# Performance work log

Hardware: AMD Instinct MI355X
Metric: run time of the kernel (lower is better)

## Reference

```python
import jax, jax.numpy as jnp
import numpy as np

D = 512      # d_model
P = 128      # proj_len
H = 8        # nhead
MID = 24     # middle_dim (hardcoded in module)
HD = MID // H    # head_dim = 3
HDV = D // H     # head_dim_v = 64
SCALE = HD ** -0.5   # scaling == pscaling since head_dim == phead_dim


def setup_inputs() -> dict:
    key = jax.random.key(0)
    ks = jax.random.split(key, 12)
    L, B = 2048, 16
    def w(k, o, i):
        return jax.random.normal(k, (o, i), jnp.float32) * 0.02
    def b(o):
        return jnp.zeros((o,), jnp.float32)
    return {
        "x": jax.random.normal(ks[0], (L, B, D), jnp.float32),
        "px": jax.random.normal(ks[1], (P, B, D), jnp.float32),
        "mask": jax.random.randint(ks[2], (B, L), 0, 2).astype(bool),
        "Wpq": w(ks[3], MID, D), "bpq": b(MID),
        "Wq": w(ks[4], MID, D), "bq": b(MID),
        "Wql": w(ks[5], P * H, D), "bql": b(P * H),
        "Wpk": w(ks[6], MID, D), "bpk": b(MID),
        "Wpv": w(ks[7], D, D), "bpv": b(D),
        "Wk": w(ks[8], MID, D), "bk": b(MID),
        "Wv": w(ks[9], D, D), "bv": b(D),
        "Wo": w(ks[10], D, D), "bo": b(D),
        "gamma": jnp.ones((D,), jnp.float32),
        "beta": jnp.zeros((D,), jnp.float32),
    }


def _layernorm(x, g, b, eps=1e-5):
    m = x.mean(-1, keepdims=True)
    v = ((x - m) ** 2).mean(-1, keepdims=True)
    return (x - m) / jnp.sqrt(v + eps) * g + b


def reference(x, px, mask, Wpq, bpq, Wq, bq, Wql, bql, Wpk, bpk, Wpv, bpv,
              Wk, bk, Wv, bv, Wo, bo, gamma, beta):
    L, B, _ = x.shape
    BH = B * H
    # ---- stage 1: compress length L -> P via projected attention ----
    pk = (x @ Wpk.T + bpk).reshape(L, BH, HD)     # [L, BH, hd]
    pv = (x @ Wpv.T + bpv).reshape(L, BH, HDV)    # [L, BH, hdv]
    pq = (px @ Wpq.T + bpq).reshape(P, BH, HD) * SCALE
    pqk = jnp.einsum('pnh,lnh->npl', pq, pk)      # [BH, P, L]
    pqk = pqk.reshape(B, H, P, L)
    pqk = jnp.where(mask[:, None, None, :], -jnp.inf, pqk).reshape(BH, P, L)
    pqk = jax.nn.softmax(pqk, axis=-1)            # dropout1 omitted (eval)
    pc = jnp.einsum('npl,lnv->npv', pqk, pv)      # [BH, P, hdv]
    pc = pc.transpose(1, 0, 2).reshape(P, B, D)   # compressed context
    # ---- stage 2: attention within compressed length P ----
    q_len = (x @ Wql.T + bql).reshape(L, BH, P).transpose(1, 0, 2)  # [BH, L, P]
    k = (pc @ Wk.T + bk).reshape(P, BH, HD).transpose(1, 0, 2)      # [BH, P, hd]
    v = (pc @ Wv.T + bv).reshape(P, BH, HDV).transpose(1, 0, 2)     # [BH, P, hdv]
    q = ((pc @ Wq.T + bq) * SCALE).reshape(P, BH, HD).transpose(1, 0, 2)
    aw = jax.nn.softmax(q @ k.transpose(0, 2, 1), axis=-1)  # [BH, P, P], dropout2 omitted
    attn = aw @ v                                            # [BH, P, hdv]
    attn = attn.transpose(1, 0, 2).reshape(P, B, D)
    attn = _layernorm(attn, gamma, beta)
    attn = attn.reshape(P, BH, HDV).transpose(1, 0, 2)       # [BH, P, hdv]
    # ---- stage 3: re-expand P -> L via learned length softmax ----
    ql = jax.nn.softmax(q_len, axis=-1)                      # dropout3 omitted
    out = (ql @ attn).transpose(1, 0, 2).reshape(L, B, D)
    return (out @ Wo.T + bo, pc)
```

## Files before the change

kernel.cpp:

```cpp
#include <hip/hip_runtime.h>
#include <cstdint>

#define L_    2048
#define B_    16
#define D_    512
#define P_    128
#define H_    8
#define MID_  24
#define HD_   3
#define HDV_  64
#define BH_   128
#define SCALE_ 0.57735026918962576f
#define S1C   4
#define S1L   (L_ / S1C)

typedef short  short8  __attribute__((ext_vector_type(8)));
typedef short  short4v __attribute__((ext_vector_type(4)));
typedef float  f32x4   __attribute__((ext_vector_type(4)));

__device__ __forceinline__ short f2bf(float f) {
    unsigned u = __builtin_bit_cast(unsigned, f);
    unsigned r = (u + 0x7fffu + ((u >> 16) & 1u)) >> 16;
    return (short)(unsigned short)r;
}

__device__ __forceinline__ float block_reduce_sum_256(float v, volatile float* scratch) {
#pragma unroll
    for (int o = 32; o > 0; o >>= 1) v += __shfl_down(v, o, 64);
    int wid = threadIdx.x >> 6;
    if ((threadIdx.x & 63) == 0) scratch[wid] = v;
    __syncthreads();
    if (threadIdx.x == 0) scratch[4] = scratch[0] + scratch[1] + scratch[2] + scratch[3];
    __syncthreads();
    return scratch[4];
}

__global__ __launch_bounds__(256) void cvt_bf16(
    const float* __restrict__ src, short* __restrict__ dst, int n4)
{
    int i = blockIdx.x * 256 + threadIdx.x;
    if (i < n4) {
        float4 v = reinterpret_cast<const float4*>(src)[i];
        short4v o;
        o[0] = f2bf(v.x); o[1] = f2bf(v.y); o[2] = f2bf(v.z); o[3] = f2bf(v.w);
        reinterpret_cast<short4v*>(dst)[i] = o;
    }
}

__global__ __launch_bounds__(256) void gemm_bias(
    const float* __restrict__ A, const float* __restrict__ W,
    const float* __restrict__ bias, float* __restrict__ C,
    int M, int N, int K, float scale)
{
    __shared__ float As[32][36];
    __shared__ float Ws[64][36];
    const int t    = threadIdx.x;
    const int row0 = blockIdx.y * 32;
    const int col0 = blockIdx.x * 64;
    const int ty = t >> 4;
    const int tx = t & 15;
    const int lr  = t >> 3;
    const int lc4 = (t & 7) * 4;

    float acc[2][4] = {{0.f,0.f,0.f,0.f},{0.f,0.f,0.f,0.f}};

    for (int kk0 = 0; kk0 < K; kk0 += 32) {
        {
            float4 a = *reinterpret_cast<const float4*>(&A[(size_t)(row0 + lr) * K + kk0 + lc4]);
            *reinterpret_cast<float4*>(&As[lr][lc4]) = a;
        }
#pragma unroll
        for (int i = 0; i < 2; ++i) {
            int wr   = i * 32 + lr;
            int wcol = col0 + wr;
            float4 w = make_float4(0.f, 0.f, 0.f, 0.f);
            if (wcol < N)
                w = *reinterpret_cast<const float4*>(&W[(size_t)wcol * K + kk0 + lc4]);
            *reinterpret_cast<float4*>(&Ws[wr][lc4]) = w;
        }
        __syncthreads();
#pragma unroll
        for (int k4 = 0; k4 < 8; ++k4) {
            float4 a0 = *reinterpret_cast<const float4*>(&As[ty * 2][k4 * 4]);
            float4 a1 = *reinterpret_cast<const float4*>(&As[ty * 2 + 1][k4 * 4]);
#pragma unroll
            for (int ci = 0; ci < 4; ++ci) {
                float4 w = *reinterpret_cast<const float4*>(&Ws[ci * 16 + tx][k4 * 4]);
                acc[0][ci] += a0.x * w.x + a0.y * w.y + a0.z * w.z + a0.w * w.w;
                acc[1][ci] += a1.x * w.x + a1.y * w.y + a1.z * w.z + a1.w * w.w;
            }
        }
        __syncthreads();
    }
#pragma unroll
    for (int ri = 0; ri < 2; ++ri) {
        int r = row0 + ty * 2 + ri;
#pragma unroll
        for (int ci = 0; ci < 4; ++ci) {
            int c = col0 + ci * 16 + tx;
            if (c < N) C[(size_t)r * N + c] = (acc[ri][ci] + bias[c]) * scale;
        }
    }
}

__global__ __launch_bounds__(256) void gemm_bias2(
    const float* __restrict__ A,
    const float* __restrict__ W0, const float* __restrict__ b0, float* __restrict__ C0, float s0,
    const float* __restrict__ W1, const float* __restrict__ b1, float* __restrict__ C1, float s1,
    int M, int N, int K)
{
    const float* W    = blockIdx.z ? W1 : W0;
    const float* bias = blockIdx.z ? b1 : b0;
    float*       C    = blockIdx.z ? C1 : C0;
    const float scale = blockIdx.z ? s1 : s0;

    __shared__ float As[32][36];
    __shared__ float Ws[64][36];
    const int t    = threadIdx.x;
    const int row0 = blockIdx.y * 32;
    const int col0 = blockIdx.x * 64;
    const int ty = t >> 4;
    const int tx = t & 15;
    const int lr  = t >> 3;
    const int lc4 = (t & 7) * 4;

    float acc[2][4] = {{0.f,0.f,0.f,0.f},{0.f,0.f,0.f,0.f}};

    for (int kk0 = 0; kk0 < K; kk0 += 32) {
        {
            float4 a = *reinterpret_cast<const float4*>(&A[(size_t)(row0 + lr) * K + kk0 + lc4]);
            *reinterpret_cast<float4*>(&As[lr][lc4]) = a;
        }
#pragma unroll
        for (int i = 0; i < 2; ++i) {
            int wr   = i * 32 + lr;
            int wcol = col0 + wr;
            float4 w = make_float4(0.f, 0.f, 0.f, 0.f);
            if (wcol < N)
                w = *reinterpret_cast<const float4*>(&W[(size_t)wcol * K + kk0 + lc4]);
            *reinterpret_cast<float4*>(&Ws[wr][lc4]) = w;
        }
        __syncthreads();
#pragma unroll
        for (int k4 = 0; k4 < 8; ++k4) {
            float4 a0 = *reinterpret_cast<const float4*>(&As[ty * 2][k4 * 4]);
            float4 a1 = *reinterpret_cast<const float4*>(&As[ty * 2 + 1][k4 * 4]);
#pragma unroll
            for (int ci = 0; ci < 4; ++ci) {
                float4 w = *reinterpret_cast<const float4*>(&Ws[ci * 16 + tx][k4 * 4]);
                acc[0][ci] += a0.x * w.x + a0.y * w.y + a0.z * w.z + a0.w * w.w;
                acc[1][ci] += a1.x * w.x + a1.y * w.y + a1.z * w.z + a1.w * w.w;
            }
        }
        __syncthreads();
    }
#pragma unroll
    for (int ri = 0; ri < 2; ++ri) {
        int r = row0 + ty * 2 + ri;
#pragma unroll
        for (int ci = 0; ci < 4; ++ci) {
            int c = col0 + ci * 16 + tx;
            if (c < N) C[(size_t)r * N + c] = (acc[ri][ci] + bias[c]) * scale;
        }
    }
}

__global__ __launch_bounds__(256) void gemm_mfma_bt(
    const float* __restrict__ A, const short* __restrict__ Wb,
    const float* __restrict__ bias, float* __restrict__ C,
    int M, int N, int K)
{
    __shared__ __align__(16) short As[128][40];
    __shared__ __align__(16) short Bs[64][40];
    const int t    = threadIdx.x;
    const int w    = t >> 6;
    const int lane = t & 63;
    const int q    = lane >> 4;
    const int l16  = lane & 15;
    const int row0 = blockIdx.y * 128;
    const int col0 = blockIdx.x * 64;

    const int ar = t >> 1;
    const int ac = (t & 1) * 16;
    const int br = t >> 2;
    const int bc = (t & 3) * 8;

    const f32x4 z = {0.f, 0.f, 0.f, 0.f};
    f32x4 acc[2][4];
#pragma unroll
    for (int i = 0; i < 2; ++i)
#pragma unroll
        for (int j = 0; j < 4; ++j) acc[i][j] = z;

    for (int kk = 0; kk < K; kk += 32) {
        {
            const float4* ap = reinterpret_cast<const float4*>(&A[(size_t)(row0 + ar) * K + kk + ac]);
            float4 v0 = ap[0], v1 = ap[1], v2 = ap[2], v3 = ap[3];
            short8 s0, s1;
            s0[0]=f2bf(v0.x); s0[1]=f2bf(v0.y); s0[2]=f2bf(v0.z); s0[3]=f2bf(v0.w);
            s0[4]=f2bf(v1.x); s0[5]=f2bf(v1.y); s0[6]=f2bf(v1.z); s0[7]=f2bf(v1.w);
            s1[0]=f2bf(v2.x); s1[1]=f2bf(v2.y); s1[2]=f2bf(v2.z); s1[3]=f2bf(v2.w);
            s1[4]=f2bf(v3.x); s1[5]=f2bf(v3.y); s1[6]=f2bf(v3.z); s1[7]=f2bf(v3.w);
            *reinterpret_cast<short8*>(&As[ar][ac])     = s0;
            *reinterpret_cast<short8*>(&As[ar][ac + 8]) = s1;
        }
        *reinterpret_cast<short8*>(&Bs[br][bc]) =
            *reinterpret_cast<const short8*>(&Wb[(size_t)(col0 + br) * K + kk + bc]);
        __syncthreads();

        short8 af[2], bf[4];
#pragma unroll
        for (int i = 0; i < 2; ++i)
            af[i] = *reinterpret_cast<const short8*>(&As[32 * w + i * 16 + l16][q * 8]);
#pragma unroll
        for (int ct = 0; ct < 4; ++ct)
            bf[ct] = *reinterpret_cast<const short8*>(&Bs[ct * 16 + l16][q * 8]);
#pragma unroll
        for (int i = 0; i < 2; ++i)
#pragma unroll
            for (int ct = 0; ct < 4; ++ct)
                acc[i][ct] = __builtin_amdgcn_mfma_f32_16x16x32_bf16(af[i], bf[ct], acc[i][ct], 0, 0, 0);
        __syncthreads();
    }

#pragma unroll
    for (int i = 0; i < 2; ++i) {
#pragma unroll
        for (int ct = 0; ct < 4; ++ct) {
            int col = col0 + ct * 16 + l16;
            float bv = bias[col];
#pragma unroll
            for (int r = 0; r < 4; ++r) {
                int row = row0 + 32 * w + i * 16 + q * 4 + r;
                C[(size_t)row * N + col] = acc[i][ct][r] + bv;
            }
        }
    }
}

template<bool BF16OUT>
__global__ __launch_bounds__(256) void gemm_bb(
    const short* __restrict__ Ab, const short* __restrict__ Wb,
    const float* __restrict__ bias, void* __restrict__ Cout,
    int M, int N, int K)
{
    __shared__ __align__(16) short As[128][40];
    __shared__ __align__(16) short Bs[128][40];
    const int t    = threadIdx.x;
    const int w    = t >> 6;
    const int lane = t & 63;
    const int q    = lane >> 4;
    const int l16  = lane & 15;
    const int row0 = blockIdx.y * 128;
    const int col0 = blockIdx.x * 128;

    const int sr = t >> 1;
    const int sc = (t & 1) * 16;

    const f32x4 z = {0.f, 0.f, 0.f, 0.f};
    f32x4 acc[2][8];
#pragma unroll
    for (int i = 0; i < 2; ++i)
#pragma unroll
        for (int j = 0; j < 8; ++j) acc[i][j] = z;

    for (int kk = 0; kk < K; kk += 32) {
        {
            const short* ap = &Ab[(size_t)(row0 + sr) * K + kk + sc];
            *reinterpret_cast<short8*>(&As[sr][sc])     = *reinterpret_cast<const short8*>(ap);
            *reinterpret_cast<short8*>(&As[sr][sc + 8]) = *reinterpret_cast<const short8*>(ap + 8);
            const short* bp = &Wb[(size_t)(col0 + sr) * K + kk + sc];
            *reinterpret_cast<short8*>(&Bs[sr][sc])     = *reinterpret_cast<const short8*>(bp);
            *reinterpret_cast<short8*>(&Bs[sr][sc + 8]) = *reinterpret_cast<const short8*>(bp + 8);
        }
        __syncthreads();

        short8 af[2], bf[8];
#pragma unroll
        for (int i = 0; i < 2; ++i)
            af[i] = *reinterpret_cast<const short8*>(&As[32 * w + i * 16 + l16][q * 8]);
#pragma unroll
        for (int ct = 0; ct < 8; ++ct)
            bf[ct] = *reinterpret_cast<const short8*>(&Bs[ct * 16 + l16][q * 8]);
#pragma unroll
        for (int i = 0; i < 2; ++i)
#pragma unroll
            for (int ct = 0; ct < 8; ++ct)
                acc[i][ct] = __builtin_amdgcn_mfma_f32_16x16x32_bf16(af[i], bf[ct], acc[i][ct], 0, 0, 0);
        __syncthreads();
    }

#pragma unroll
    for (int i = 0; i < 2; ++i) {
#pragma unroll
        for (int ct = 0; ct < 8; ++ct) {
            int col = col0 + ct * 16 + l16;
            float bv = bias[col];
#pragma unroll
            for (int r = 0; r < 4; ++r) {
                int row = row0 + 32 * w + i * 16 + q * 4 + r;
                float v = acc[i][ct][r] + bv;
                if (BF16OUT)
                    ((short*)Cout)[(size_t)row * N + col] = f2bf(v);
                else
                    ((float*)Cout)[(size_t)row * N + col] = v;
            }
        }
    }
}

__global__ __launch_bounds__(512) void stage1_split(
    const float* __restrict__ pk, const float* __restrict__ pq,
    const short* __restrict__ pvb, const int* __restrict__ mask,
    float* __restrict__ pc, float* __restrict__ sumtot)
{
    __shared__ float pkt[S1L * 3];
    __shared__ float mka[S1L];
    __shared__ __align__(16) short As[P_][40];
    __shared__ __align__(16) short pvt[32][68];

    const int t = threadIdx.x;
    const int n = blockIdx.x;
    const int c = blockIdx.y;
    const int lbase = c * S1L;
    const int b = n >> 3;
    const int h = n & 7;

    {
        const int l = t;
        const float* pp = &pk[((size_t)(lbase + l) * BH_ + n) * HD_];
        pkt[l * 3 + 0] = pp[0];
        pkt[l * 3 + 1] = pp[1];
        pkt[l * 3 + 2] = pp[2];
        mka[l] = mask[b * L_ + lbase + l] ? -1e30f : 0.f;
    }

    const int p   = t >> 2;
    const int pl8 = (t & 3) * 8;
    const float pq0 = pq[((size_t)p * B_ + b) * MID_ + h * HD_ + 0];
    const float pq1 = pq[((size_t)p * B_ + b) * MID_ + h * HD_ + 1];
    const float pq2 = pq[((size_t)p * B_ + b) * MID_ + h * HD_ + 2];
    __syncthreads();

    const int lane = t & 63;
    const int w    = t >> 6;
    const int q    = lane >> 4;
    const int l16  = lane & 15;
    const int svl  = t >> 4;
    const int svc  = (t & 15) * 4;

    float psum = 0.f;
    const f32x4 z = {0.f, 0.f, 0.f, 0.f};
    f32x4 acc[4] = {z, z, z, z};

    for (int kt = 0; kt < S1L / 32; ++kt) {
        *reinterpret_cast<short4v*>(&pvt[svl][svc]) =
            *reinterpret_cast<const short4v*>(&pvb[((size_t)(lbase + kt * 32 + svl) * BH_ + n) * HDV_ + svc]);
        {
            const float* pb = &pkt[(kt * 32 + pl8) * 3];
            float kv[24], mk[8];
#pragma unroll
            for (int j = 0; j < 6; ++j)
                *reinterpret_cast<float4*>(&kv[j * 4]) = *reinterpret_cast<const float4*>(pb + j * 4);
            *reinterpret_cast<float4*>(&mk[0]) = *reinterpret_cast<const float4*>(&mka[kt * 32 + pl8]);
            *reinterpret_cast<float4*>(&mk[4]) = *reinterpret_cast<const float4*>(&mka[kt * 32 + pl8 + 4]);
            short8 a8;
#pragma unroll
            for (int j = 0; j < 8; ++j) {
                float s = pq0 * kv[j * 3] + pq1 * kv[j * 3 + 1] + pq2 * kv[j * 3 + 2] + mk[j];
                float e = __expf(s);
                psum += e;
                a8[j] = f2bf(e);
            }
            *reinterpret_cast<short8*>(&As[p][pl8]) = a8;
        }
        __syncthreads();

        short8 af = *reinterpret_cast<const short8*>(&As[w * 16 + l16][q * 8]);
#pragma unroll
        for (int ct = 0; ct < 4; ++ct) {
            short8 bf;
#pragma unroll
            for (int j = 0; j < 8; ++j) bf[j] = pvt[q * 8 + j][ct * 16 + l16];
            acc[ct] = __builtin_amdgcn_mfma_f32_16x16x32_bf16(af, bf, acc[ct], 0, 0, 0);
        }
        __syncthreads();
    }

    psum += __shfl_xor(psum, 1, 64);
    psum += __shfl_xor(psum, 2, 64);
    if ((t & 3) == 0) unsafeAtomicAdd(&sumtot[n * P_ + p], psum);

#pragma unroll
    for (int ct = 0; ct < 4; ++ct) {
        int dv = ct * 16 + l16;
#pragma unroll
        for (int r = 0; r < 4; ++r) {
            int pr = w * 16 + q * 4 + r;
            unsafeAtomicAdd(&pc[((size_t)(pr * B_ + b)) * D_ + h * HDV_ + dv], acc[ct][r]);
        }
    }
}

__global__ __launch_bounds__(256) void normalize_pc(
    float* __restrict__ pc, const float* __restrict__ sumtot)
{
    int i = blockIdx.x * 256 + threadIdx.x;
    float4 v = reinterpret_cast<float4*>(pc)[i];
    int flat = i * 4;
    int pb = flat >> 9;
    int d  = flat & 511;
    int p = pb >> 4, b = pb & 15, h = d >> 6;
    float s = 1.f / sumtot[(b * H_ + h) * P_ + p];
    v.x *= s; v.y *= s; v.z *= s; v.w *= s;
    reinterpret_cast<float4*>(pc)[i] = v;
}

__global__ __launch_bounds__(256) void stage2_attn(
    const float* __restrict__ qtmp, const float* __restrict__ ktmp,
    const float* __restrict__ vtmp, float* __restrict__ apre)
{
    __shared__ float S[32][132];
    __shared__ float ks[128][4];
    __shared__ float qs[32][4];
    __shared__ float vs[128][64];
    const int t  = threadIdx.x;
    const int n  = blockIdx.x;
    const int b  = n >> 3;
    const int h  = n & 7;
    const int p0 = blockIdx.y * 32;

    if (t < 128) {
        const float* kr = &ktmp[(size_t)(t * B_ + b) * MID_ + h * HD_];
        ks[t][0] = kr[0]; ks[t][1] = kr[1]; ks[t][2] = kr[2];
    } else if (t < 160) {
        int r = t - 128;
        const float* qr = &qtmp[(size_t)((p0 + r) * B_ + b) * MID_ + h * HD_];
        qs[r][0] = qr[0]; qs[r][1] = qr[1]; qs[r][2] = qr[2];
    }
#pragma unroll
    for (int j = 0; j < 8; ++j) {
        int idx = t + j * 256;
        int r = idx >> 4, c4 = (idx & 15) * 4;
        *reinterpret_cast<float4*>(&vs[r][c4]) =
            *reinterpret_cast<const float4*>(&vtmp[(size_t)(r * B_ + b) * D_ + h * HDV_ + c4]);
    }
    __syncthreads();

    {
        const int c  = t & 127;
        const int rg = t >> 7;
        float k0 = ks[c][0], k1 = ks[c][1], k2 = ks[c][2];
#pragma unroll
        for (int i = 0; i < 16; ++i) {
            int r = rg * 16 + i;
            S[r][c] = qs[r][0] * k0 + qs[r][1] * k1 + qs[r][2] * k2;
        }
    }
    __syncthreads();

    {
        const int srow = t >> 3;
        const int c0   = (t & 7) * 16;
        float mx = -1e30f;
#pragma unroll
        for (int i = 0; i < 16; ++i) mx = fmaxf(mx, S[srow][c0 + i]);
        mx = fmaxf(mx, __shfl_xor(mx, 1, 64));
        mx = fmaxf(mx, __shfl_xor(mx, 2, 64));
        mx = fmaxf(mx, __shfl_xor(mx, 4, 64));
        float e[16];
        float sum = 0.f;
#pragma unroll
        for (int i = 0; i < 16; ++i) { e[i] = __expf(S[srow][c0 + i] - mx); sum += e[i]; }
        sum += __shfl_xor(sum, 1, 64);
        sum += __shfl_xor(sum, 2, 64);
        sum += __shfl_xor(sum, 4, 64);
        float inv = 1.f / sum;
#pragma unroll
        for (int i = 0; i < 16; ++i) S[srow][c0 + i] = e[i] * inv;
    }
    __syncthreads();

    {
        const int dv = t & 63;
        const int pg = t >> 6;
        float acc[8] = {0.f,0.f,0.f,0.f,0.f,0.f,0.f,0.f};
        for (int pp = 0; pp < 128; pp += 4) {
            float v0 = vs[pp + 0][dv], v1 = vs[pp + 1][dv];
            float v2 = vs[pp + 2][dv], v3 = vs[pp + 3][dv];
#pragma unroll
            for (int pi = 0; pi < 8; ++pi) {
                const float4 s4 = *reinterpret_cast<const float4*>(&S[pg * 8 + pi][pp]);
                acc[pi] = fmaf(s4.x, v0, fmaf(s4.y, v1, fmaf(s4.z, v2, fmaf(s4.w, v3, acc[pi]))));
            }
        }
#pragma unroll
        for (int pi = 0; pi < 8; ++pi)
            apre[(size_t)((p0 + pg * 8 + pi) * B_ + b) * D_ + h * HDV_ + dv] = acc[pi];
    }
}

__global__ __launch_bounds__(256) void layernorm_t(
    const float* __restrict__ apre, const float* __restrict__ gamma,
    const float* __restrict__ beta, short* __restrict__ attnT2)
{
    __shared__ float red[8];
    const int t   = threadIdx.x;
    const int row = blockIdx.x;
    const int p   = row >> 4;
    const int b   = row & 15;
    float v0 = apre[(size_t)row * D_ + t];
    float v1 = apre[(size_t)row * D_ + 256 + t];
    float mean = block_reduce_sum_256(v0 + v1, red) * (1.f / D_);
    float d0 = v0 - mean, d1 = v1 - mean;
    float var  = block_reduce_sum_256(d0 * d0 + d1 * d1, red) * (1.f / D_);
    float rstd = rsqrtf(var + 1e-5f);
#pragma unroll
    for (int j = 0; j < 2; ++j) {
        int d = t + j * 256;
        int h = d >> 6, dv = d & 63;
        float v = (j ? d1 : d0) * rstd * gamma[d] + beta[d];
        attnT2[(((size_t)(b * H_ + h)) * HDV_ + dv) * P_ + p] = f2bf(v);
    }
}

__global__ __launch_bounds__(512, 4) void score_softmax(
    const short* __restrict__ xb, const short* __restrict__ Wqlb,
    const float* __restrict__ bql, short* __restrict__ probsT)
{
    __shared__ __align__(16) short As[128][40];
    __shared__ __align__(16) short Bs[128][40];
    __shared__ float reds[128][4];

    const int t    = threadIdx.x;
    const int l0   = blockIdx.x * 128;
    const int h    = blockIdx.y;
    const int lane = t & 63;
    const int w    = t >> 6;
    const int q    = lane >> 4;
    const int l16  = lane & 15;
    const int rg   = w & 3;
    const int ch   = w >> 2;
    const int sar  = t >> 2;
    const int sac  = (t & 3) * 8;

    const f32x4 z = {0.f, 0.f, 0.f, 0.f};
    f32x4 acc[2][4];
#pragma unroll
    for (int i = 0; i < 2; ++i)
#pragma unroll
        for (int j = 0; j < 4; ++j) acc[i][j] = z;

    for (int kk = 0; kk < D_; kk += 32) {
        *reinterpret_cast<short8*>(&As[sar][sac]) =
            *reinterpret_cast<const short8*>(&xb[(size_t)(l0 + sar) * D_ + kk + sac]);
        *reinterpret_cast<short8*>(&Bs[sar][sac]) =
            *reinterpret_cast<const short8*>(&Wqlb[(size_t)(h * P_ + sar) * D_ + kk + sac]);
        __syncthreads();

        short8 af[2], bf[4];
#pragma unroll
        for (int i = 0; i < 2; ++i)
            af[i] = *reinterpret_cast<const short8*>(&Bs[rg * 32 + i * 16 + l16][q * 8]);
#pragma unroll
        for (int ct = 0; ct < 4; ++ct)
            bf[ct] = *reinterpret_cast<const short8*>(&As[ch * 64 + ct * 16 + l16][q * 8]);
#pragma unroll
        for (int i = 0; i < 2; ++i)
#pragma unroll
            for (int ct = 0; ct < 4; ++ct)
                acc[i][ct] = __builtin_amdgcn_mfma_f32_16x16x32_bf16(af[i], bf[ct], acc[i][ct], 0, 0, 0);
        __syncthreads();
    }

    {
        float bv[2][4];
#pragma unroll
        for (int i = 0; i < 2; ++i)
#pragma unroll
            for (int r = 0; r < 4; ++r)
                bv[i][r] = bql[h * P_ + rg * 32 + i * 16 + q * 4 + r];
#pragma unroll
        for (int i = 0; i < 2; ++i)
#pragma unroll
            for (int ct = 0; ct < 4; ++ct)
#pragma unroll
                for (int r = 0; r < 4; ++r)
                    acc[i][ct][r] += bv[i][r];
    }

    float e[4][2][4];
#pragma unroll
    for (int ct = 0; ct < 4; ++ct) {
        float s = 0.f;
#pragma unroll
        for (int i = 0; i < 2; ++i)
#pragma unroll
            for (int r = 0; r < 4; ++r) {
                float v = __expf(acc[i][ct][r]);
                e[ct][i][r] = v;
                s += v;
            }
        s += __shfl_xor(s, 16, 64);
        s += __shfl_xor(s, 32, 64);
        if (q == 0) reds[ch * 64 + ct * 16 + l16][rg] = s;
    }
    __syncthreads();

#pragma unroll
    for (int ct = 0; ct < 4; ++ct) {
        const int lc = ch * 64 + ct * 16 + l16;
        float S   = reds[lc][0] + reds[lc][1] + reds[lc][2] + reds[lc][3];
        float inv = 1.f / S;

        const int lrow = (l0 + ch * 64 + ct * 16) >> 4;
        const int b    = l16;
        short* dst = &probsT[((size_t)b * L_ + lrow) * (P_ * H_) + h * P_ + rg * 32 + q * 4];
#pragma unroll
        for (int i = 0; i < 2; ++i) {
            short4v o;
#pragma unroll
            for (int r = 0; r < 4; ++r)
                o[r] = f2bf(e[ct][i][r] * inv);
            *reinterpret_cast<short4v*>(dst + i * 16) = o;
        }
    }
}

__global__ __launch_bounds__(256) void expand_y(
    const short* __restrict__ probsT, const short* __restrict__ attnT2,
    short* __restrict__ yb)
{
    __shared__ __align__(16) short As[128][40];
    __shared__ __align__(16) short Bt[64][136];
    const int t    = threadIdx.x;
    const int b    = blockIdx.x >> 4;
    const int l0   = (blockIdx.x & 15) * 128;
    const int h    = blockIdx.y;
    const int lane = t & 63;
    const int w    = t >> 6;
    const int q    = lane >> 4;
    const int l16  = lane & 15;

    {
        int r = t >> 2, c = (t & 3) * 32;
        const short* src = &attnT2[(((size_t)(b * H_ + h)) * HDV_ + r) * P_ + c];
#pragma unroll
        for (int j = 0; j < 4; ++j)
            *reinterpret_cast<short8*>(&Bt[r][c + j * 8]) =
                *reinterpret_cast<const short8*>(src + j * 8);
    }

    const int ar = t >> 1;
    const int ac = (t & 1) * 16;
    const f32x4 z = {0.f, 0.f, 0.f, 0.f};
    f32x4 acc[2][4];
#pragma unroll
    for (int i = 0; i < 2; ++i)
#pragma unroll
        for (int j = 0; j < 4; ++j) acc[i][j] = z;

    for (int ks = 0; ks < 4; ++ks) {
        const int kk = ks * 32;
        const short* ap = &probsT[((size_t)b * L_ + l0 + ar) * (P_ * H_) + h * P_ + kk + ac];
        *reinterpret_cast<short8*>(&As[ar][ac])     = *reinterpret_cast<const short8*>(ap);
        *reinterpret_cast<short8*>(&As[ar][ac + 8]) = *reinterpret_cast<const short8*>(ap + 8);
        __syncthreads();

        short8 af[2], bf[4];
#pragma unroll
        for (int i = 0; i < 2; ++i)
            af[i] = *reinterpret_cast<const short8*>(&As[32 * w + i * 16 + l16][q * 8]);
#pragma unroll
        for (int ct = 0; ct < 4; ++ct)
            bf[ct] = *reinterpret_cast<const short8*>(&Bt[ct * 16 + l16][kk + q * 8]);
#pragma unroll
        for (int i = 0; i < 2; ++i)
#pragma unroll
            for (int ct = 0; ct < 4; ++ct)
                acc[i][ct] = __builtin_amdgcn_mfma_f32_16x16x32_bf16(af[i], bf[ct], acc[i][ct], 0, 0, 0);
        __syncthreads();
    }

#pragma unroll
    for (int i = 0; i < 2; ++i) {
#pragma unroll
        for (int ct = 0; ct < 4; ++ct) {
            int col = ct * 16 + l16;
#pragma unroll
            for (int r = 0; r < 4; ++r) {
                int row = 32 * w + i * 16 + q * 4 + r;
                yb[((size_t)(l0 + row) * B_ + b) * D_ + h * HDV_ + col] = f2bf(acc[i][ct][r]);
            }
        }
    }
}

extern "C" void kernel_launch(void* const* d_in, const int* in_sizes, int n_in,
                              void* d_out, int out_size, void* d_ws, size_t ws_size,
                              hipStream_t stream)
{
    const float* x     = (const float*)d_in[0];
    const float* px    = (const float*)d_in[1];
    const int*   mask  = (const int*)d_in[2];
    const float* Wpq   = (const float*)d_in[3];
    const float* bpq   = (const float*)d_in[4];
    const float* Wq    = (const float*)d_in[5];
    const float* bq    = (const float*)d_in[6];
    const float* Wql   = (const float*)d_in[7];
    const float* bql   = (const float*)d_in[8];
    const float* Wpk   = (const float*)d_in[9];
    const float* bpk   = (const float*)d_in[10];
    const float* Wpv   = (const float*)d_in[11];
    const float* bpv   = (const float*)d_in[12];
    const float* Wk    = (const float*)d_in[13];
    const float* bk    = (const float*)d_in[14];
    const float* Wv    = (const float*)d_in[15];
    const float* bv    = (const float*)d_in[16];
    const float* Wo    = (const float*)d_in[17];
    const float* bo    = (const float*)d_in[18];
    const float* gamma = (const float*)d_in[19];
    const float* beta  = (const float*)d_in[20];

    float* out = (float*)d_out;
    float* pc  = out + (size_t)L_ * B_ * D_;

    float* ws    = (float*)d_ws;
    float* pk    = ws;
    float* pq    = pk    + 786432;
    float* ktmp  = pq    + 49152;
    float* qtmp  = ktmp  + 49152;
    float* vtmp  = qtmp  + 49152;
    float* apre  = vtmp  + 1048576;
    short* Wpvb  = (short*)(apre + 1048576);
    short* Wob   = Wpvb + 262144;
    short* Wqlb  = Wob  + 262144;
    short* Wvb   = Wqlb + 524288;
    short* xb    = Wvb  + 262144;
    short* pvb   = xb   + 16777216;
    float* sumtot = (float*)(pvb + 16777216);
    short* yb    = xb;
    short* attnT2 = (short*)pk;
    short* probsT = (short*)d_out;

    const int MLB = L_ * B_;
    const int MPB = P_ * B_;

    cvt_bf16<<<dim3(256),   256, 0, stream>>>(Wpv, Wpvb, D_*D_/4);
    cvt_bf16<<<dim3(256),   256, 0, stream>>>(Wo,  Wob,  D_*D_/4);
    cvt_bf16<<<dim3(512),   256, 0, stream>>>(Wql, Wqlb, P_*H_*D_/4);
    cvt_bf16<<<dim3(256),   256, 0, stream>>>(Wv,  Wvb,  D_*D_/4);
    cvt_bf16<<<dim3(16384), 256, 0, stream>>>(x,   xb,   MLB*D_/4);

    hipMemsetAsync(pc, 0, (size_t)P_ * B_ * D_ * sizeof(float), stream);
    hipMemsetAsync(sumtot, 0, (size_t)BH_ * P_ * sizeof(float), stream);

    gemm_bias<<<dim3(1, MLB / 32), 256, 0, stream>>>(x,  Wpk, bpk, pk, MLB, MID_, D_, 1.f);
    gemm_bias<<<dim3(1, MPB / 32), 256, 0, stream>>>(px, Wpq, bpq, pq, MPB, MID_, D_, SCALE_);
    gemm_bb<true><<<dim3(D_ / 128, MLB / 128), 256, 0, stream>>>(xb, Wpvb, bpv, pvb, MLB, D_, D_);
    stage1_split<<<dim3(BH_, S1C), 512, 0, stream>>>(pk, pq, pvb, mask, pc, sumtot);
    normalize_pc<<<dim3(P_ * B_ * D_ / 4 / 256), 256, 0, stream>>>(pc, sumtot);
    gemm_bias2<<<dim3(1, MPB / 32, 2), 256, 0, stream>>>(pc, Wk, bk, ktmp, 1.f,
                                                          Wq, bq, qtmp, SCALE_, MPB, MID_, D_);
    gemm_mfma_bt<<<dim3(D_ / 64, MPB / 128), 256, 0, stream>>>(pc, Wvb, bv, vtmp, MPB, D_, D_);
    stage2_attn<<<dim3(BH_, 4), 256, 0, stream>>>(qtmp, ktmp, vtmp, apre);
    layernorm_t<<<dim3(MPB), 256, 0, stream>>>(apre, gamma, beta, attnT2);
    score_softmax<<<dim3(MLB / 128, H_), 512, 0, stream>>>(xb, Wqlb, bql, probsT);
    expand_y<<<dim3(B_ * 16, H_), 256, 0, stream>>>(probsT, attnT2, yb);
    gemm_bb<false><<<dim3(D_ / 128, MLB / 128), 256, 0, stream>>>(yb, Wob, bo, out, MLB, D_, D_);
}
```

Baseline: 517.6 us.

## Swizzle LDS tiles and remap block indices for XCD-aware scheduling

```diff
diff --git a/kernel.cpp b/kernel.cpp
--- a/kernel.cpp
+++ b/kernel.cpp
@@ -24,6 +24,10 @@
     return (short)(unsigned short)r;
 }
 
+__device__ __forceinline__ int swz_off(int row, int chunk) {
+    return row * 32 + ((chunk ^ ((row >> 1) & 3)) << 3);
+}
+
 __device__ __forceinline__ float block_reduce_sum_256(float v, volatile float* scratch) {
 #pragma unroll
     for (int o = 32; o > 0; o >>= 1) v += __shfl_down(v, o, 64);
@@ -244,44 +248,51 @@
     const float* __restrict__ bias, void* __restrict__ Cout,
     int M, int N, int K)
 {
-    __shared__ __align__(16) short As[128][40];
-    __shared__ __align__(16) short Bs[128][40];
+    __shared__ __align__(16) short As[128 * 32];
+    __shared__ __align__(16) short Bs[128 * 32];
     const int t    = threadIdx.x;
     const int w    = t >> 6;
     const int lane = t & 63;
     const int q    = lane >> 4;
     const int l16  = lane & 15;
-    const int row0 = blockIdx.y * 128;
-    const int col0 = blockIdx.x * 128;
-
-    const int sr = t >> 1;
-    const int sc = (t & 1) * 16;
+
+    const int gid  = blockIdx.x;
+    const int nct  = N >> 7;
+    const int xcd  = gid & 7;
+    const int j    = gid >> 3;
+    const int row0 = (xcd + 8 * (j / nct)) * 128;
+    const int col0 = (j % nct) * 128;
+
+    const int sr  = t >> 1;
+    const int sc0 = (t & 1) * 2;
+    const int offS0 = swz_off(sr, sc0);
+    const int offS1 = swz_off(sr, sc0 + 1);
 
     const f32x4 z = {0.f, 0.f, 0.f, 0.f};
     f32x4 acc[2][8];
 #pragma unroll
     for (int i = 0; i < 2; ++i)
 #pragma unroll
-        for (int j = 0; j < 8; ++j) acc[i][j] = z;
+        for (int jj = 0; jj < 8; ++jj) acc[i][jj] = z;
 
     for (int kk = 0; kk < K; kk += 32) {
         {
-            const short* ap = &Ab[(size_t)(row0 + sr) * K + kk + sc];
-            *reinterpret_cast<short8*>(&As[sr][sc])     = *reinterpret_cast<const short8*>(ap);
-            *reinterpret_cast<short8*>(&As[sr][sc + 8]) = *reinterpret_cast<const short8*>(ap + 8);
-            const short* bp = &Wb[(size_t)(col0 + sr) * K + kk + sc];
-            *reinterpret_cast<short8*>(&Bs[sr][sc])     = *reinterpret_cast<const short8*>(bp);
-            *reinterpret_cast<short8*>(&Bs[sr][sc + 8]) = *reinterpret_cast<const short8*>(bp + 8);
+            const short* ap = &Ab[(size_t)(row0 + sr) * K + kk + sc0 * 8];
+            *reinterpret_cast<short8*>(&As[offS0]) = *reinterpret_cast<const short8*>(ap);
+            *reinterpret_cast<short8*>(&As[offS1]) = *reinterpret_cast<const short8*>(ap + 8);
+            const short* bp = &Wb[(size_t)(col0 + sr) * K + kk + sc0 * 8];
+            *reinterpret_cast<short8*>(&Bs[offS0]) = *reinterpret_cast<const short8*>(bp);
+            *reinterpret_cast<short8*>(&Bs[offS1]) = *reinterpret_cast<const short8*>(bp + 8);
         }
         __syncthreads();
 
         short8 af[2], bf[8];
 #pragma unroll
         for (int i = 0; i < 2; ++i)
-            af[i] = *reinterpret_cast<const short8*>(&As[32 * w + i * 16 + l16][q * 8]);
+            af[i] = *reinterpret_cast<const short8*>(&As[swz_off(32 * w + i * 16 + l16, q)]);
 #pragma unroll
         for (int ct = 0; ct < 8; ++ct)
-            bf[ct] = *reinterpret_cast<const short8*>(&Bs[ct * 16 + l16][q * 8]);
+            bf[ct] = *reinterpret_cast<const short8*>(&Bs[swz_off(ct * 16 + l16, q)]);
 #pragma unroll
         for (int i = 0; i < 2; ++i)
 #pragma unroll
@@ -528,13 +539,17 @@
     const short* __restrict__ xb, const short* __restrict__ Wqlb,
     const float* __restrict__ bql, short* __restrict__ probsT)
 {
-    __shared__ __align__(16) short As[128][40];
-    __shared__ __align__(16) short Bs[128][40];
+    __shared__ __align__(16) short As[128 * 32];
+    __shared__ __align__(16) short Bs[128 * 32];
     __shared__ float reds[128][4];
 
     const int t    = threadIdx.x;
-    const int l0   = blockIdx.x * 128;
-    const int h    = blockIdx.y;
+    const int gid  = blockIdx.x;
+    const int xcd  = gid & 7;
+    const int j    = gid >> 3;
+    const int h    = j & 7;
+    const int l0   = (xcd + 8 * (j >> 3)) * 128;
+
     const int lane = t & 63;
     const int w    = t >> 6;
     const int q    = lane >> 4;
@@ -542,29 +557,30 @@
     const int rg   = w & 3;
     const int ch   = w >> 2;
     const int sar  = t >> 2;
-    const int sac  = (t & 3) * 8;
+    const int sch  = t & 3;
+    const int soff = swz_off(sar, sch);
 
     const f32x4 z = {0.f, 0.f, 0.f, 0.f};
     f32x4 acc[2][4];
 #pragma unroll
     for (int i = 0; i < 2; ++i)
 #pragma unroll
-        for (int j = 0; j < 4; ++j) acc[i][j] = z;
+        for (int jj = 0; jj < 4; ++jj) acc[i][jj] = z;
 
     for (int kk = 0; kk < D_; kk += 32) {
-        *reinterpret_cast<short8*>(&As[sar][sac]) =
-            *reinterpret_cast<const short8*>(&xb[(size_t)(l0 + sar) * D_ + kk + sac]);
-        *reinterpret_cast<short8*>(&Bs[sar][sac]) =
-            *reinterpret_cast<const short8*>(&Wqlb[(size_t)(h * P_ + sar) * D_ + kk + sac]);
+        *reinterpret_cast<short8*>(&As[soff]) =
+            *reinterpret_cast<const short8*>(&xb[(size_t)(l0 + sar) * D_ + kk + sch * 8]);
+        *reinterpret_cast<short8*>(&Bs[soff]) =
+            *reinterpret_cast<const short8*>(&Wqlb[(size_t)(h * P_ + sar) * D_ + kk + sch * 8]);
         __syncthreads();
 
         short8 af[2], bf[4];
 #pragma unroll
         for (int i = 0; i < 2; ++i)
-            af[i] = *reinterpret_cast<const short8*>(&Bs[rg * 32 + i * 16 + l16][q * 8]);
+            af[i] = *reinterpret_cast<const short8*>(&Bs[swz_off(rg * 32 + i * 16 + l16, q)]);
 #pragma unroll
         for (int ct = 0; ct < 4; ++ct)
-            bf[ct] = *reinterpret_cast<const short8*>(&As[ch * 64 + ct * 16 + l16][q * 8]);
+            bf[ct] = *reinterpret_cast<const short8*>(&As[swz_off(ch * 64 + ct * 16 + l16, q)]);
 #pragma unroll
         for (int i = 0; i < 2; ++i)
 #pragma unroll
@@ -631,7 +647,7 @@
     const short* __restrict__ probsT, const short* __restrict__ attnT2,
     short* __restrict__ yb)
 {
-    __shared__ __align__(16) short As[128][40];
+    __shared__ __align__(16) short As[128 * 32];
     __shared__ __align__(16) short Bt[64][136];
     const int t    = threadIdx.x;
     const int b    = blockIdx.x >> 4;
@@ -651,8 +667,10 @@
                 *reinterpret_cast<const short8*>(src + j * 8);
     }
 
-    const int ar = t >> 1;
-    const int ac = (t & 1) * 16;
+    const int ar  = t >> 1;
+    const int ac0 = (t & 1) * 2;
+    const int offA0 = swz_off(ar, ac0);
+    const int offA1 = swz_off(ar, ac0 + 1);
     const f32x4 z = {0.f, 0.f, 0.f, 0.f};
     f32x4 acc[2][4];
 #pragma unroll
@@ -662,15 +680,15 @@
 
     for (int ks = 0; ks < 4; ++ks) {
         const int kk = ks * 32;
-        const short* ap = &probsT[((size_t)b * L_ + l0 + ar) * (P_ * H_) + h * P_ + kk + ac];
-        *reinterpret_cast<short8*>(&As[ar][ac])     = *reinterpret_cast<const short8*>(ap);
-        *reinterpret_cast<short8*>(&As[ar][ac + 8]) = *reinterpret_cast<const short8*>(ap + 8);
+        const short* ap = &probsT[((size_t)b * L_ + l0 + ar) * (P_ * H_) + h * P_ + kk + ac0 * 8];
+        *reinterpret_cast<short8*>(&As[offA0]) = *reinterpret_cast<const short8*>(ap);
+        *reinterpret_cast<short8*>(&As[offA1]) = *reinterpret_cast<const short8*>(ap + 8);
         __syncthreads();
 
         short8 af[2], bf[4];
 #pragma unroll
         for (int i = 0; i < 2; ++i)
-            af[i] = *reinterpret_cast<const short8*>(&As[32 * w + i * 16 + l16][q * 8]);
+            af[i] = *reinterpret_cast<const short8*>(&As[swz_off(32 * w + i * 16 + l16, q)]);
 #pragma unroll
         for (int ct = 0; ct < 4; ++ct)
             bf[ct] = *reinterpret_cast<const short8*>(&Bt[ct * 16 + l16][kk + q * 8]);
@@ -757,7 +775,7 @@
 
     gemm_bias<<<dim3(1, MLB / 32), 256, 0, stream>>>(x,  Wpk, bpk, pk, MLB, MID_, D_, 1.f);
     gemm_bias<<<dim3(1, MPB / 32), 256, 0, stream>>>(px, Wpq, bpq, pq, MPB, MID_, D_, SCALE_);
-    gemm_bb<true><<<dim3(D_ / 128, MLB / 128), 256, 0, stream>>>(xb, Wpvb, bpv, pvb, MLB, D_, D_);
+    gemm_bb<true><<<dim3((MLB / 128) * (D_ / 128)), 256, 0, stream>>>(xb, Wpvb, bpv, pvb, MLB, D_, D_);
     stage1_split<<<dim3(BH_, S1C), 512, 0, stream>>>(pk, pq, pvb, mask, pc, sumtot);
     normalize_pc<<<dim3(P_ * B_ * D_ / 4 / 256), 256, 0, stream>>>(pc, sumtot);
     gemm_bias2<<<dim3(1, MPB / 32, 2), 256, 0, stream>>>(pc, Wk, bk, ktmp, 1.f,
@@ -765,7 +783,7 @@
     gemm_mfma_bt<<<dim3(D_ / 64, MPB / 128), 256, 0, stream>>>(pc, Wvb, bv, vtmp, MPB, D_, D_);
     stage2_attn<<<dim3(BH_, 4), 256, 0, stream>>>(qtmp, ktmp, vtmp, apre);
     layernorm_t<<<dim3(MPB), 256, 0, stream>>>(apre, gamma, beta, attnT2);
-    score_softmax<<<dim3(MLB / 128, H_), 512, 0, stream>>>(xb, Wqlb, bql, probsT);
+    score_softmax<<<dim3((MLB / 128) * H_), 512, 0, stream>>>(xb, Wqlb, bql, probsT);
     expand_y<<<dim3(B_ * 16, H_), 256, 0, stream>>>(probsT, attnT2, yb);
-    gemm_bb<false><<<dim3(D_ / 128, MLB / 128), 256, 0, stream>>>(yb, Wob, bo, out, MLB, D_, D_);
-}
+    gemm_bb<false><<<dim3((MLB / 128) * (D_ / 128)), 256, 0, stream>>>(yb, Wob, bo, out, MLB, D_, D_);
+}
```

New measurement: 490.7 us. -5.2%, faster.
